# Kernel optimization log

Hardware: AMD Instinct MI355X
Metric: run time of the kernel (lower is better)

The kernel has to match this reference:

```python
import jax, jax.numpy as jnp
import numpy as np

N_NODES = 100000
N_EDGES = 800000
IN_FEATS = 128
HIDDEN = 128
NUM_CLASSES = 10
NUM_GRAPHS = 128
BN_EPS = 1e-5


def setup_inputs() -> dict:
    key = jax.random.key(0)
    ks = jax.random.split(key, 16)
    s = 0.05  # weight init scale
    return {
        "x": jax.random.normal(ks[0], (N_NODES, IN_FEATS), dtype=jnp.float32),
        "edge_index": jax.random.randint(ks[1], (2, N_EDGES), 0, N_NODES, dtype=jnp.int64),
        "batch": jnp.sort(jax.random.randint(ks[2], (N_NODES,), 0, NUM_GRAPHS, dtype=jnp.int64)),
        # conv1 MLP: Linear(in,h) -> ReLU -> Linear(h,h)
        "W1a": jax.random.normal(ks[3], (IN_FEATS, HIDDEN), dtype=jnp.float32) * s,
        "b1a": jnp.zeros((HIDDEN,), dtype=jnp.float32),
        "W1b": jax.random.normal(ks[4], (HIDDEN, HIDDEN), dtype=jnp.float32) * s,
        "b1b": jnp.zeros((HIDDEN,), dtype=jnp.float32),
        "gamma1": jnp.ones((HIDDEN,), dtype=jnp.float32),
        "beta1": jnp.zeros((HIDDEN,), dtype=jnp.float32),
        # conv2 MLP
        "W2a": jax.random.normal(ks[5], (HIDDEN, HIDDEN), dtype=jnp.float32) * s,
        "b2a": jnp.zeros((HIDDEN,), dtype=jnp.float32),
        "W2b": jax.random.normal(ks[6], (HIDDEN, HIDDEN), dtype=jnp.float32) * s,
        "b2b": jnp.zeros((HIDDEN,), dtype=jnp.float32),
        "gamma2": jnp.ones((HIDDEN,), dtype=jnp.float32),
        "beta2": jnp.zeros((HIDDEN,), dtype=jnp.float32),
        # final classifier
        "Wlin": jax.random.normal(ks[7], (HIDDEN, NUM_CLASSES), dtype=jnp.float32) * s,
        "blin": jnp.zeros((NUM_CLASSES,), dtype=jnp.float32),
    }


def _gin_conv(x, edge_index, Wa, ba, Wb, bb, eps=0.0):
    # GINConv: MLP((1+eps)*x_i + sum_{j->i} x_j); scatter-add over edges
    src, dst = edge_index[0], edge_index[1]
    agg = jax.ops.segment_sum(x[src], dst, num_segments=N_NODES)
    h = (1.0 + eps) * x + agg
    h = jax.nn.relu(h @ Wa + ba) @ Wb + bb
    return h


def _batch_norm(x, gamma, beta):
    # training-mode BN over the node dim (biased variance, as in torch)
    mean = jnp.mean(x, axis=0)
    var = jnp.mean(jnp.square(x - mean), axis=0)
    return (x - mean) * jax.lax.rsqrt(var + BN_EPS) * gamma + beta


def reference(x, edge_index, batch, W1a, b1a, W1b, b1b, gamma1, beta1,
              W2a, b2a, W2b, b2b, gamma2, beta2, Wlin, blin):
    h = _gin_conv(x, edge_index, W1a, b1a, W1b, b1b)
    h = jax.nn.relu(_batch_norm(h, gamma1, beta1))
    # dropout: eval mode -> identity
    h = _gin_conv(h, edge_index, W2a, b2a, W2b, b2b)
    h = jax.nn.relu(_batch_norm(h, gamma2, beta2))
    # global mean pool per graph
    summed = jax.ops.segment_sum(h, batch, num_segments=NUM_GRAPHS)
    counts = jax.ops.segment_sum(jnp.ones((h.shape[0],), h.dtype), batch, num_segments=NUM_GRAPHS)
    pooled = summed / jnp.maximum(counts, 1.0)[:, None]  # [G, H]
    logits = pooled @ Wlin + blin
    return jax.nn.log_softmax(logits, axis=1)
```

## Files before the change

### kernel.cpp

```cpp
#include <hip/hip_runtime.h>

#define N_NODES 100000
#define N_EDGESC 800000
#define HID 128
#define NGRAPH 128
#define BN_EPS 1e-5f
#define NREP 32
#define PS 136
#define MLP_BLOCKS ((N_NODES + 63) / 64)

#define PBLK 256
#define PCHUNK 3125
#define NCOARSE 196
#define HISTN (NCOARSE * PBLK)
#define HSCAN_BLOCKS (HISTN / 1024)

typedef __bf16 bf16x8 __attribute__((ext_vector_type(8)));
typedef float f32x4 __attribute__((ext_vector_type(4)));

__device__ inline unsigned short f2bf(float f) {
    unsigned int u = __float_as_uint(f);
    unsigned int r = u + 0x7FFFu + ((u >> 16) & 1u);
    return (unsigned short)(r >> 16);
}
__device__ inline float b2f(unsigned short u) {
    return __uint_as_float(((unsigned int)u) << 16);
}


__global__ __launch_bounds__(256) void k_phist(const int* __restrict__ dst,
                                               int* __restrict__ hist)
{
    __shared__ int h[NCOARSE];
    if (threadIdx.x < NCOARSE) h[threadIdx.x] = 0;
    __syncthreads();
    int base = blockIdx.x * PCHUNK;
    for (int i = threadIdx.x; i < PCHUNK; i += 256)
        atomicAdd(&h[dst[base + i] >> 9], 1);
    __syncthreads();
    if (threadIdx.x < NCOARSE)
        hist[threadIdx.x * PBLK + blockIdx.x] = h[threadIdx.x];
}

__global__ __launch_bounds__(256) void k_scan_block(int* __restrict__ a,
    int* __restrict__ bsum, int n)
{
    __shared__ int ts[256];
    int base = blockIdx.x * 1024 + threadIdx.x * 4;
    int v[4], s = 0;
    #pragma unroll
    for (int i = 0; i < 4; ++i) {
        int idx = base + i;
        v[i] = (idx < n) ? a[idx] : 0;
        s += v[i];
    }
    ts[threadIdx.x] = s;
    __syncthreads();
    for (int d = 1; d < 256; d <<= 1) {
        int t = (threadIdx.x >= d) ? ts[threadIdx.x - d] : 0;
        __syncthreads();
        ts[threadIdx.x] += t;
        __syncthreads();
    }
    int run = ts[threadIdx.x] - s;
    #pragma unroll
    for (int i = 0; i < 4; ++i) {
        int idx = base + i;
        if (idx < n) a[idx] = run;
        run += v[i];
    }
    if (threadIdx.x == 255) bsum[blockIdx.x] = ts[255];
}

__global__ void k_scan_top(int* __restrict__ bsum, int nb)
{
    int run = 0;
    for (int i = 0; i < nb; ++i) { int t = bsum[i]; bsum[i] = run; run += t; }
}

__global__ __launch_bounds__(256) void k_scan_add(int* __restrict__ a,
    const int* __restrict__ bsum, int n)
{
    int i = blockIdx.x * 256 + threadIdx.x;
    if (i < n) a[i] += bsum[i >> 10];
}

__global__ __launch_bounds__(256) void k_pscatter(const int* __restrict__ src,
    const int* __restrict__ dst, const int* __restrict__ hist,
    unsigned int* __restrict__ pk1)
{
    __shared__ int cur[NCOARSE];
    if (threadIdx.x < NCOARSE)
        cur[threadIdx.x] = hist[threadIdx.x * PBLK + blockIdx.x];
    __syncthreads();
    int base = blockIdx.x * PCHUNK;
    for (int i = threadIdx.x; i < PCHUNK; i += 256) {
        int s = src[base + i], d = dst[base + i];
        int p = atomicAdd(&cur[d >> 9], 1);
        pk1[p] = ((unsigned int)s << 9) | (unsigned int)(d & 511);
    }
}

__global__ __launch_bounds__(256) void k_psort(const unsigned int* __restrict__ pk1,
    const int* __restrict__ hist, int* __restrict__ eidx, int* __restrict__ off)
{
    __shared__ int h[512], cur[512], ts[256];
    const int b = blockIdx.x;
    const int e0 = hist[b * PBLK];
    const int e1 = (b == NCOARSE - 1) ? N_EDGESC : hist[(b + 1) * PBLK];
    const int cnt = e1 - e0;
    h[threadIdx.x] = 0; h[threadIdx.x + 256] = 0;
    __syncthreads();
    for (int i = threadIdx.x; i < cnt; i += 256)
        atomicAdd(&h[pk1[e0 + i] & 511], 1);
    __syncthreads();
    int v0 = h[threadIdx.x * 2], v1 = h[threadIdx.x * 2 + 1];
    int s = v0 + v1;
    ts[threadIdx.x] = s;
    __syncthreads();
    for (int d = 1; d < 256; d <<= 1) {
        int t = (threadIdx.x >= d) ? ts[threadIdx.x - d] : 0;
        __syncthreads();
        ts[threadIdx.x] += t;
        __syncthreads();
    }
    int run = e0 + ts[threadIdx.x] - s;
    int n0 = b * 512 + threadIdx.x * 2;
    cur[threadIdx.x * 2]     = run;
    cur[threadIdx.x * 2 + 1] = run + v0;
    if (n0     <= N_NODES) off[n0]     = run;
    if (n0 + 1 <= N_NODES) off[n0 + 1] = run + v0;
    __syncthreads();
    for (int i = threadIdx.x; i < cnt; i += 256) {
        unsigned int u = pk1[e0 + i];
        int p = atomicAdd(&cur[u & 511], 1);
        eidx[p] = (int)(u >> 9);
    }
}

__global__ __launch_bounds__(256) void k_cvt(const float* __restrict__ X,
    unsigned short* __restrict__ Y, int n4)
{
    int i = blockIdx.x * 256 + threadIdx.x;
    if (i < n4) {
        float4 v = ((const float4*)X)[i];
        ((ushort4*)Y)[i] = make_ushort4(f2bf(v.x), f2bf(v.y), f2bf(v.z), f2bf(v.w));
    }
}

__global__ __launch_bounds__(256) void k_wcvt4(const float* __restrict__ Wa,
    const float* __restrict__ Wb, const float* __restrict__ Wc,
    const float* __restrict__ Wd, unsigned short* __restrict__ WT)
{
    int idx = blockIdx.x * 256 + threadIdx.x;
    int mat = idx >> 14, w = idx & 16383;
    int k = w >> 7, n = w & 127;
    const float* W = (mat == 0) ? Wa : (mat == 1) ? Wb : (mat == 2) ? Wc : Wd;
    WT[mat * 16384 + n * 128 + k] = f2bf(W[w]);
}

template<bool BN>
__device__ inline void acc_row(float* acc, uint4 v,
                               const float* sc, const float* sh)
{
    unsigned int u[4] = {v.x, v.y, v.z, v.w};
    #pragma unroll
    for (int j = 0; j < 4; ++j) {
        float lo = b2f((unsigned short)u[j]);
        float hi = b2f((unsigned short)(u[j] >> 16));
        if (BN) {
            lo = fmaxf(lo * sc[2*j]   + sh[2*j],   0.f);
            hi = fmaxf(hi * sc[2*j+1] + sh[2*j+1], 0.f);
        }
        acc[2*j]   += lo;
        acc[2*j+1] += hi;
    }
}

template<bool BN>
__global__ __launch_bounds__(256) void k_gather(
    const unsigned short* __restrict__ X, const float* __restrict__ SC,
    const int* __restrict__ off, const int* __restrict__ eidx,
    unsigned short* __restrict__ OUT, int M)
{
    int n = blockIdx.x * 16 + (threadIdx.x >> 4);
    if (n >= M) return;
    const int lane = threadIdx.x & 15;
    const size_t co = (size_t)lane * 8;

    float sc[8], sh[8];
    if (BN) {
        *(float4*)&sc[0] = ((const float4*)SC)[lane * 2];
        *(float4*)&sc[4] = ((const float4*)SC)[lane * 2 + 1];
        *(float4*)&sh[0] = ((const float4*)SC)[32 + lane * 2];
        *(float4*)&sh[4] = ((const float4*)SC)[32 + lane * 2 + 1];
    }

    float acc[8] = {0.f, 0.f, 0.f, 0.f, 0.f, 0.f, 0.f, 0.f};
    acc_row<BN>(acc, *(const uint4*)(X + (size_t)n * HID + co), sc, sh);

    int k = off[n], kend = off[n + 1];
    for (; k + 7 < kend; k += 8) {
        uint4 v0 = *(const uint4*)(X + (size_t)eidx[k]   * HID + co);
        uint4 v1 = *(const uint4*)(X + (size_t)eidx[k+1] * HID + co);
        uint4 v2 = *(const uint4*)(X + (size_t)eidx[k+2] * HID + co);
        uint4 v3 = *(const uint4*)(X + (size_t)eidx[k+3] * HID + co);
        uint4 v4 = *(const uint4*)(X + (size_t)eidx[k+4] * HID + co);
        uint4 v5 = *(const uint4*)(X + (size_t)eidx[k+5] * HID + co);
        uint4 v6 = *(const uint4*)(X + (size_t)eidx[k+6] * HID + co);
        uint4 v7 = *(const uint4*)(X + (size_t)eidx[k+7] * HID + co);
        acc_row<BN>(acc, v0, sc, sh); acc_row<BN>(acc, v1, sc, sh);
        acc_row<BN>(acc, v2, sc, sh); acc_row<BN>(acc, v3, sc, sh);
        acc_row<BN>(acc, v4, sc, sh); acc_row<BN>(acc, v5, sc, sh);
        acc_row<BN>(acc, v6, sc, sh); acc_row<BN>(acc, v7, sc, sh);
    }
    for (; k + 3 < kend; k += 4) {
        uint4 v0 = *(const uint4*)(X + (size_t)eidx[k]   * HID + co);
        uint4 v1 = *(const uint4*)(X + (size_t)eidx[k+1] * HID + co);
        uint4 v2 = *(const uint4*)(X + (size_t)eidx[k+2] * HID + co);
        uint4 v3 = *(const uint4*)(X + (size_t)eidx[k+3] * HID + co);
        acc_row<BN>(acc, v0, sc, sh); acc_row<BN>(acc, v1, sc, sh);
        acc_row<BN>(acc, v2, sc, sh); acc_row<BN>(acc, v3, sc, sh);
    }
    for (; k < kend; ++k) {
        uint4 v = *(const uint4*)(X + (size_t)eidx[k] * HID + co);
        acc_row<BN>(acc, v, sc, sh);
    }

    uint4 o;
    o.x = (unsigned int)f2bf(acc[0]) | ((unsigned int)f2bf(acc[1]) << 16);
    o.y = (unsigned int)f2bf(acc[2]) | ((unsigned int)f2bf(acc[3]) << 16);
    o.z = (unsigned int)f2bf(acc[4]) | ((unsigned int)f2bf(acc[5]) << 16);
    o.w = (unsigned int)f2bf(acc[6]) | ((unsigned int)f2bf(acc[7]) << 16);
    *(uint4*)(OUT + (size_t)n * HID + co) = o;
}

__global__ __launch_bounds__(256) void k_mlp(
    const unsigned short* __restrict__ A,
    const unsigned short* __restrict__ WTa, const float* __restrict__ ba,
    const unsigned short* __restrict__ WTb, const float* __restrict__ bb,
    unsigned short* __restrict__ Cb, float* __restrict__ Srep, int M)
{
    __shared__ unsigned short Abuf[64 * PS];
    __shared__ unsigned short Hbuf[64 * PS];

    const int tid  = threadIdx.x;
    const int wave = tid >> 6;
    const int lane = tid & 63;
    const int m    = lane & 15;
    const int quad = lane >> 4;
    const int rowbase = blockIdx.x * 64;

    bf16x8 WA[2][4], WB[2][4];
    float bav[2], bbv[2];
    #pragma unroll
    for (int n0 = 0; n0 < 2; ++n0) {
        const int col = (wave * 2 + n0) * 16 + m;
        const size_t cb = (size_t)col * HID + quad * 8;
        #pragma unroll
        for (int kk = 0; kk < 4; ++kk) {
            WA[n0][kk] = *(const bf16x8*)(WTa + cb + kk * 32);
            WB[n0][kk] = *(const bf16x8*)(WTb + cb + kk * 32);
        }
        bav[n0] = ba[col];
        bbv[n0] = bb[col];
    }

    {
        const uint4* Ag = (const uint4*)(A + (size_t)rowbase * HID);
        #pragma unroll
        for (int i = 0; i < 4; ++i) {
            int u = tid + i * 256;
            uint4 v = Ag[u];
            int r = u >> 4, c = u & 15;
            *(uint4*)(Abuf + r * PS + c * 8) = v;
        }
    }
    __syncthreads();

    f32x4 acc[4][2];
    #pragma unroll
    for (int rg = 0; rg < 4; ++rg)
        #pragma unroll
        for (int n0 = 0; n0 < 2; ++n0) acc[rg][n0] = {0.f, 0.f, 0.f, 0.f};
    #pragma unroll
    for (int rg = 0; rg < 4; ++rg) {
        #pragma unroll
        for (int kk = 0; kk < 4; ++kk) {
            bf16x8 af = *(const bf16x8*)(Abuf + (rg*16 + m) * PS + quad*8 + kk*32);
            acc[rg][0] = __builtin_amdgcn_mfma_f32_16x16x32_bf16(af, WA[0][kk], acc[rg][0], 0, 0, 0);
            acc[rg][1] = __builtin_amdgcn_mfma_f32_16x16x32_bf16(af, WA[1][kk], acc[rg][1], 0, 0, 0);
        }
    }

    #pragma unroll
    for (int rg = 0; rg < 4; ++rg)
        #pragma unroll
        for (int n0 = 0; n0 < 2; ++n0)
            #pragma unroll
            for (int i = 0; i < 4; ++i)
                Hbuf[(rg*16 + quad*4 + i) * PS + (wave*2 + n0)*16 + m] =
                    f2bf(fmaxf(acc[rg][n0][i] + bav[n0], 0.f));
    __syncthreads();

    #pragma unroll
    for (int rg = 0; rg < 4; ++rg)
        #pragma unroll
        for (int n0 = 0; n0 < 2; ++n0) acc[rg][n0] = {0.f, 0.f, 0.f, 0.f};
    #pragma unroll
    for (int rg = 0; rg < 4; ++rg) {
        #pragma unroll
        for (int kk = 0; kk < 4; ++kk) {
            bf16x8 hf = *(const bf16x8*)(Hbuf + (rg*16 + m) * PS + quad*8 + kk*32);
            acc[rg][0] = __builtin_amdgcn_mfma_f32_16x16x32_bf16(hf, WB[0][kk], acc[rg][0], 0, 0, 0);
            acc[rg][1] = __builtin_amdgcn_mfma_f32_16x16x32_bf16(hf, WB[1][kk], acc[rg][1], 0, 0, 0);
        }
    }

    const bool full = (rowbase + 64 <= M);
    float s[2] = {0.f, 0.f}, s2[2] = {0.f, 0.f};
    #pragma unroll
    for (int rg = 0; rg < 4; ++rg) {
        #pragma unroll
        for (int n0 = 0; n0 < 2; ++n0) {
            #pragma unroll
            for (int i = 0; i < 4; ++i) {
                float v = acc[rg][n0][i] + bbv[n0];
                if (full || rowbase + rg*16 + quad*4 + i < M) { s[n0] += v; s2[n0] += v*v; }
                Abuf[(rg*16 + quad*4 + i) * PS + (wave*2 + n0)*16 + m] = f2bf(v);
            }
        }
    }
    __syncthreads();

    #pragma unroll
    for (int i = 0; i < 4; ++i) {
        int u = tid + i * 256;
        int r = u >> 4, c = u & 15;
        uint4 v = *(const uint4*)(Abuf + r * PS + c * 8);
        int g = rowbase + r;
        if (g < M) *(uint4*)(Cb + (size_t)g * HID + c * 8) = v;
    }

    #pragma unroll
    for (int n0 = 0; n0 < 2; ++n0) {
        s[n0]  += __shfl_xor(s[n0], 16, 64);
        s[n0]  += __shfl_xor(s[n0], 32, 64);
        s2[n0] += __shfl_xor(s2[n0], 16, 64);
        s2[n0] += __shfl_xor(s2[n0], 32, 64);
    }
    if (quad == 0) {
        float* R = Srep + (size_t)((blockIdx.x * 4 + wave) & (NREP - 1)) * 256;
        #pragma unroll
        for (int n0 = 0; n0 < 2; ++n0) {
            int col = (wave * 2 + n0) * 16 + m;
            atomicAdd(&R[col], s[n0]);
            atomicAdd(&R[128 + col], s2[n0]);
        }
    }
}

__global__ void k_bnfinalize(const float* __restrict__ Srep,
    const float* __restrict__ gamma, const float* __restrict__ beta,
    float* __restrict__ SC, int M)
{
    int f = threadIdx.x;
    float s = 0.f, s2 = 0.f;
    for (int r = 0; r < NREP; ++r) {
        s += Srep[r * 256 + f];
        s2 += Srep[r * 256 + 128 + f];
    }
    float mean = s / (float)M;
    float var = s2 / (float)M - mean * mean;
    var = fmaxf(var, 0.f);
    float sc = gamma[f] * rsqrtf(var + BN_EPS);
    SC[f] = sc;
    SC[HID + f] = beta[f] - mean * sc;
}

__global__ void k_bounds(const int* __restrict__ batch, int* __restrict__ gstart)
{
    int g = threadIdx.x;
    int lo = 0, hi = N_NODES;
    while (lo < hi) {
        int mid = (lo + hi) >> 1;
        if (batch[mid] < g) lo = mid + 1; else hi = mid;
    }
    gstart[g] = lo;
    if (g == 0) gstart[NGRAPH] = N_NODES;
}

__global__ __launch_bounds__(256) void k_pool(const unsigned short* __restrict__ H,
    const float* __restrict__ SC, const int* __restrict__ gstart,
    float* __restrict__ P)
{
    int g = blockIdx.x >> 4, part = blockIdx.x & 15;
    int beg = gstart[g], end = gstart[g + 1];
    int f = threadIdx.x & 127, half = threadIdx.x >> 7;
    float sc = SC[f], sh = SC[HID + f];
    float s = 0.f;
    for (int r = beg + part * 2 + half; r < end; r += 32)
        s += fmaxf(b2f(H[(size_t)r * HID + f]) * sc + sh, 0.f);
    __shared__ float ls[256];
    ls[threadIdx.x] = s;
    __syncthreads();
    if (threadIdx.x < 128)
        atomicAdd(&P[g * HID + threadIdx.x], ls[threadIdx.x] + ls[threadIdx.x + 128]);
}

__global__ void k_head(const float* __restrict__ P, const int* __restrict__ gstart,
    const float* __restrict__ Wlin, const float* __restrict__ blin,
    float* __restrict__ out)
{
    int g = blockIdx.x;
    int l = threadIdx.x;
    float inv = 1.f / (float)max(gstart[g + 1] - gstart[g], 1);
    float p0 = P[(size_t)g * HID + l] * inv;
    float p1 = P[(size_t)g * HID + 64 + l] * inv;
    float lg[10];
    #pragma unroll
    for (int c = 0; c < 10; ++c) {
        float v = p0 * Wlin[l * 10 + c] + p1 * Wlin[(64 + l) * 10 + c];
        #pragma unroll
        for (int off = 32; off > 0; off >>= 1) v += __shfl_down(v, off);
        lg[c] = v;
    }
    if (l == 0) {
        float mx = -1e30f;
        #pragma unroll
        for (int c = 0; c < 10; ++c) { lg[c] += blin[c]; mx = fmaxf(mx, lg[c]); }
        float s = 0.f;
        #pragma unroll
        for (int c = 0; c < 10; ++c) s += expf(lg[c] - mx);
        float lse = mx + logf(s);
        #pragma unroll
        for (int c = 0; c < 10; ++c) out[g * 10 + c] = lg[c] - lse;
    }
}

extern "C" void kernel_launch(void* const* d_in, const int* in_sizes, int n_in,
                              void* d_out, int out_size, void* d_ws, size_t ws_size,
                              hipStream_t stream)
{
    const float* x    = (const float*)d_in[0];
    const int*   ei   = (const int*)d_in[1];
    const int*   batch= (const int*)d_in[2];
    const float* W1a  = (const float*)d_in[3];
    const float* b1a  = (const float*)d_in[4];
    const float* W1b  = (const float*)d_in[5];
    const float* b1b  = (const float*)d_in[6];
    const float* g1   = (const float*)d_in[7];
    const float* be1  = (const float*)d_in[8];
    const float* W2a  = (const float*)d_in[9];
    const float* b2a  = (const float*)d_in[10];
    const float* W2b  = (const float*)d_in[11];
    const float* b2b  = (const float*)d_in[12];
    const float* g2   = (const float*)d_in[13];
    const float* be2  = (const float*)d_in[14];
    const float* Wl   = (const float*)d_in[15];
    const float* bl   = (const float*)d_in[16];
    float* out = (float*)d_out;

    const int* src = ei;
    const int* dst = ei + N_EDGESC;

    const size_t NM = (size_t)N_NODES * HID;
    char* wsb = (char*)d_ws;
    unsigned short* Ab  = (unsigned short*)wsb;
    unsigned short* Yb  = Ab + NM;
    unsigned short* Xb  = Yb + NM;
    float* Srep1 = (float*)(Xb + NM);
    float* Srep2 = Srep1 + NREP * 256;
    float* SC1  = Srep2 + NREP * 256;
    float* SC2  = SC1 + 256;
    float* P    = SC2 + 256;
    unsigned short* WT = (unsigned short*)(P + (size_t)NGRAPH * HID);
    int* hist   = (int*)(WT + 4 * 16384);
    int* eidx   = hist + HISTN;
    int* off    = eidx + N_EDGESC;
    int* bsum   = off + N_NODES + 1;
    int* gstart = bsum + 64;
    unsigned int* pk1 = (unsigned int*)Xb;

    dim3 blk(256);
    const int cvtBlocks = (int)(NM / 4 + 255) / 256;
    const int gatBlocks = (N_NODES + 15) / 16;

    hipMemsetAsync(P, 0, (size_t)NGRAPH * HID * sizeof(float), stream);
    hipMemsetAsync(Srep1, 0, 2 * NREP * 256 * sizeof(float), stream);

    k_phist<<<PBLK, blk, 0, stream>>>(dst, hist);
    k_scan_block<<<HSCAN_BLOCKS, blk, 0, stream>>>(hist, bsum, HISTN);
    k_scan_top<<<1, 1, 0, stream>>>(bsum, HSCAN_BLOCKS);
    k_scan_add<<<(HISTN + 255) / 256, blk, 0, stream>>>(hist, bsum, HISTN);
    k_pscatter<<<PBLK, blk, 0, stream>>>(src, dst, hist, pk1);
    k_psort<<<NCOARSE, blk, 0, stream>>>(pk1, hist, eidx, off);
    k_bounds<<<1, 128, 0, stream>>>(batch, gstart);

    k_cvt<<<cvtBlocks, blk, 0, stream>>>(x, Xb, (int)(NM / 4));
    k_wcvt4<<<256, blk, 0, stream>>>(W1a, W1b, W2a, W2b, WT);

    k_gather<false><<<gatBlocks, blk, 0, stream>>>(Xb, nullptr, off, eidx, Ab, N_NODES);
    k_mlp<<<MLP_BLOCKS, blk, 0, stream>>>(Ab, WT, b1a, WT + 16384, b1b, Yb, Srep1, N_NODES);
    k_bnfinalize<<<1, 128, 0, stream>>>(Srep1, g1, be1, SC1, N_NODES);

    k_gather<true><<<gatBlocks, blk, 0, stream>>>(Yb, SC1, off, eidx, Ab, N_NODES);
    k_mlp<<<MLP_BLOCKS, blk, 0, stream>>>(Ab, WT + 2 * 16384, b2a, WT + 3 * 16384, b2b, Xb, Srep2, N_NODES);
    k_bnfinalize<<<1, 128, 0, stream>>>(Srep2, g2, be2, SC2, N_NODES);

    k_pool<<<NGRAPH * 16, blk, 0, stream>>>(Xb, SC2, gstart, P);
    k_head<<<NGRAPH, 64, 0, stream>>>(P, gstart, Wl, bl, out);
}
```

Baseline: 309.5 us.

## Fuse neighbor gather into MLP kernel, aggregating directly into shared memory

```diff
diff --git a/kernel.cpp b/kernel.cpp
--- a/kernel.cpp
+++ b/kernel.cpp
@@ -7,7 +7,7 @@
 #define BN_EPS 1e-5f
 #define NREP 32
 #define PS 136
-#define MLP_BLOCKS ((N_NODES + 63) / 64)
+#define CONV_BLOCKS ((N_NODES + 63) / 64)
 
 #define PBLK 256
 #define PCHUNK 3125
@@ -178,15 +178,39 @@
 }
 
 template<bool BN>
-__global__ __launch_bounds__(256) void k_gather(
+__global__ __launch_bounds__(256) void k_conv(
     const unsigned short* __restrict__ X, const float* __restrict__ SC,
     const int* __restrict__ off, const int* __restrict__ eidx,
-    unsigned short* __restrict__ OUT, int M)
-{
-    int n = blockIdx.x * 16 + (threadIdx.x >> 4);
-    if (n >= M) return;
-    const int lane = threadIdx.x & 15;
-    const size_t co = (size_t)lane * 8;
+    const unsigned short* __restrict__ WTa, const float* __restrict__ ba,
+    const unsigned short* __restrict__ WTb, const float* __restrict__ bb,
+    unsigned short* __restrict__ Cb, float* __restrict__ Srep, int M)
+{
+    __shared__ unsigned short Abuf[64 * PS];
+    __shared__ unsigned short Hbuf[64 * PS];
+
+    const int tid  = threadIdx.x;
+    const int wave = tid >> 6;
+    const int l64  = tid & 63;
+    const int m    = l64 & 15;
+    const int quad = l64 >> 4;
+    const int grp  = tid >> 4;
+    const int lane = tid & 15;
+    const int rowbase = blockIdx.x * 64;
+
+    bf16x8 WA[2][4], WB[2][4];
+    float bav[2], bbv[2];
+    #pragma unroll
+    for (int n0 = 0; n0 < 2; ++n0) {
+        const int col = (wave * 2 + n0) * 16 + m;
+        const size_t cb = (size_t)col * HID + quad * 8;
+        #pragma unroll
+        for (int kk = 0; kk < 4; ++kk) {
+            WA[n0][kk] = *(const bf16x8*)(WTa + cb + kk * 32);
+            WB[n0][kk] = *(const bf16x8*)(WTb + cb + kk * 32);
+        }
+        bav[n0] = ba[col];
+        bbv[n0] = bb[col];
+    }
 
     float sc[8], sh[8];
     if (BN) {
@@ -196,100 +220,63 @@
         *(float4*)&sh[4] = ((const float4*)SC)[32 + lane * 2 + 1];
     }
 
-    float acc[8] = {0.f, 0.f, 0.f, 0.f, 0.f, 0.f, 0.f, 0.f};
-    acc_row<BN>(acc, *(const uint4*)(X + (size_t)n * HID + co), sc, sh);
-
-    int k = off[n], kend = off[n + 1];
-    for (; k + 7 < kend; k += 8) {
-        uint4 v0 = *(const uint4*)(X + (size_t)eidx[k]   * HID + co);
-        uint4 v1 = *(const uint4*)(X + (size_t)eidx[k+1] * HID + co);
-        uint4 v2 = *(const uint4*)(X + (size_t)eidx[k+2] * HID + co);
-        uint4 v3 = *(const uint4*)(X + (size_t)eidx[k+3] * HID + co);
-        uint4 v4 = *(const uint4*)(X + (size_t)eidx[k+4] * HID + co);
-        uint4 v5 = *(const uint4*)(X + (size_t)eidx[k+5] * HID + co);
-        uint4 v6 = *(const uint4*)(X + (size_t)eidx[k+6] * HID + co);
-        uint4 v7 = *(const uint4*)(X + (size_t)eidx[k+7] * HID + co);
-        acc_row<BN>(acc, v0, sc, sh); acc_row<BN>(acc, v1, sc, sh);
-        acc_row<BN>(acc, v2, sc, sh); acc_row<BN>(acc, v3, sc, sh);
-        acc_row<BN>(acc, v4, sc, sh); acc_row<BN>(acc, v5, sc, sh);
-        acc_row<BN>(acc, v6, sc, sh); acc_row<BN>(acc, v7, sc, sh);
-    }
-    for (; k + 3 < kend; k += 4) {
-        uint4 v0 = *(const uint4*)(X + (size_t)eidx[k]   * HID + co);
-        uint4 v1 = *(const uint4*)(X + (size_t)eidx[k+1] * HID + co);
-        uint4 v2 = *(const uint4*)(X + (size_t)eidx[k+2] * HID + co);
-        uint4 v3 = *(const uint4*)(X + (size_t)eidx[k+3] * HID + co);
-        acc_row<BN>(acc, v0, sc, sh); acc_row<BN>(acc, v1, sc, sh);
-        acc_row<BN>(acc, v2, sc, sh); acc_row<BN>(acc, v3, sc, sh);
-    }
-    for (; k < kend; ++k) {
-        uint4 v = *(const uint4*)(X + (size_t)eidx[k] * HID + co);
-        acc_row<BN>(acc, v, sc, sh);
-    }
-
-    uint4 o;
-    o.x = (unsigned int)f2bf(acc[0]) | ((unsigned int)f2bf(acc[1]) << 16);
-    o.y = (unsigned int)f2bf(acc[2]) | ((unsigned int)f2bf(acc[3]) << 16);
-    o.z = (unsigned int)f2bf(acc[4]) | ((unsigned int)f2bf(acc[5]) << 16);
-    o.w = (unsigned int)f2bf(acc[6]) | ((unsigned int)f2bf(acc[7]) << 16);
-    *(uint4*)(OUT + (size_t)n * HID + co) = o;
-}
-
-__global__ __launch_bounds__(256) void k_mlp(
-    const unsigned short* __restrict__ A,
-    const unsigned short* __restrict__ WTa, const float* __restrict__ ba,
-    const unsigned short* __restrict__ WTb, const float* __restrict__ bb,
-    unsigned short* __restrict__ Cb, float* __restrict__ Srep, int M)
-{
-    __shared__ unsigned short Abuf[64 * PS];
-    __shared__ unsigned short Hbuf[64 * PS];
-
-    const int tid  = threadIdx.x;
-    const int wave = tid >> 6;
-    const int lane = tid & 63;
-    const int m    = lane & 15;
-    const int quad = lane >> 4;
-    const int rowbase = blockIdx.x * 64;
-
-    bf16x8 WA[2][4], WB[2][4];
-    float bav[2], bbv[2];
-    #pragma unroll
-    for (int n0 = 0; n0 < 2; ++n0) {
-        const int col = (wave * 2 + n0) * 16 + m;
-        const size_t cb = (size_t)col * HID + quad * 8;
-        #pragma unroll
-        for (int kk = 0; kk < 4; ++kk) {
-            WA[n0][kk] = *(const bf16x8*)(WTa + cb + kk * 32);
-            WB[n0][kk] = *(const bf16x8*)(WTb + cb + kk * 32);
-        }
-        bav[n0] = ba[col];
-        bbv[n0] = bb[col];
-    }
-
-    {
-        const uint4* Ag = (const uint4*)(A + (size_t)rowbase * HID);
-        #pragma unroll
-        for (int i = 0; i < 4; ++i) {
-            int u = tid + i * 256;
-            uint4 v = Ag[u];
-            int r = u >> 4, c = u & 15;
-            *(uint4*)(Abuf + r * PS + c * 8) = v;
-        }
-    }
-    __syncthreads();
-
-    f32x4 acc[4][2];
+    const size_t co = (size_t)lane * 8;
+    #pragma unroll
+    for (int j = 0; j < 4; ++j) {
+        const int r = grp + j * 16;
+        const int n = rowbase + r;
+        float acc[8] = {0.f, 0.f, 0.f, 0.f, 0.f, 0.f, 0.f, 0.f};
+        if (n < M) {
+            acc_row<BN>(acc, *(const uint4*)(X + (size_t)n * HID + co), sc, sh);
+            int k = off[n], kend = off[n + 1];
+            for (; k + 7 < kend; k += 8) {
+                uint4 v0 = *(const uint4*)(X + (size_t)eidx[k]   * HID + co);
+                uint4 v1 = *(const uint4*)(X + (size_t)eidx[k+1] * HID + co);
+                uint4 v2 = *(const uint4*)(X + (size_t)eidx[k+2] * HID + co);
+                uint4 v3 = *(const uint4*)(X + (size_t)eidx[k+3] * HID + co);
+                uint4 v4 = *(const uint4*)(X + (size_t)eidx[k+4] * HID + co);
+                uint4 v5 = *(const uint4*)(X + (size_t)eidx[k+5] * HID + co);
+                uint4 v6 = *(const uint4*)(X + (size_t)eidx[k+6] * HID + co);
+                uint4 v7 = *(const uint4*)(X + (size_t)eidx[k+7] * HID + co);
+                acc_row<BN>(acc, v0, sc, sh); acc_row<BN>(acc, v1, sc, sh);
+                acc_row<BN>(acc, v2, sc, sh); acc_row<BN>(acc, v3, sc, sh);
+                acc_row<BN>(acc, v4, sc, sh); acc_row<BN>(acc, v5, sc, sh);
+                acc_row<BN>(acc, v6, sc, sh); acc_row<BN>(acc, v7, sc, sh);
+            }
+            for (; k + 3 < kend; k += 4) {
+                uint4 v0 = *(const uint4*)(X + (size_t)eidx[k]   * HID + co);
+                uint4 v1 = *(const uint4*)(X + (size_t)eidx[k+1] * HID + co);
+                uint4 v2 = *(const uint4*)(X + (size_t)eidx[k+2] * HID + co);
+                uint4 v3 = *(const uint4*)(X + (size_t)eidx[k+3] * HID + co);
+                acc_row<BN>(acc, v0, sc, sh); acc_row<BN>(acc, v1, sc, sh);
+                acc_row<BN>(acc, v2, sc, sh); acc_row<BN>(acc, v3, sc, sh);
+            }
+            for (; k < kend; ++k) {
+                uint4 v = *(const uint4*)(X + (size_t)eidx[k] * HID + co);
+                acc_row<BN>(acc, v, sc, sh);
+            }
+        }
+        uint4 o;
+        o.x = (unsigned int)f2bf(acc[0]) | ((unsigned int)f2bf(acc[1]) << 16);
+        o.y = (unsigned int)f2bf(acc[2]) | ((unsigned int)f2bf(acc[3]) << 16);
+        o.z = (unsigned int)f2bf(acc[4]) | ((unsigned int)f2bf(acc[5]) << 16);
+        o.w = (unsigned int)f2bf(acc[6]) | ((unsigned int)f2bf(acc[7]) << 16);
+        *(uint4*)(Abuf + r * PS + lane * 8) = o;
+    }
+    __syncthreads();
+
+    f32x4 acc2[4][2];
     #pragma unroll
     for (int rg = 0; rg < 4; ++rg)
         #pragma unroll
-        for (int n0 = 0; n0 < 2; ++n0) acc[rg][n0] = {0.f, 0.f, 0.f, 0.f};
+        for (int n0 = 0; n0 < 2; ++n0) acc2[rg][n0] = {0.f, 0.f, 0.f, 0.f};
     #pragma unroll
     for (int rg = 0; rg < 4; ++rg) {
         #pragma unroll
         for (int kk = 0; kk < 4; ++kk) {
             bf16x8 af = *(const bf16x8*)(Abuf + (rg*16 + m) * PS + quad*8 + kk*32);
-            acc[rg][0] = __builtin_amdgcn_mfma_f32_16x16x32_bf16(af, WA[0][kk], acc[rg][0], 0, 0, 0);
-            acc[rg][1] = __builtin_amdgcn_mfma_f32_16x16x32_bf16(af, WA[1][kk], acc[rg][1], 0, 0, 0);
+            acc2[rg][0] = __builtin_amdgcn_mfma_f32_16x16x32_bf16(af, WA[0][kk], acc2[rg][0], 0, 0, 0);
+            acc2[rg][1] = __builtin_amdgcn_mfma_f32_16x16x32_bf16(af, WA[1][kk], acc2[rg][1], 0, 0, 0);
         }
     }
 
@@ -300,20 +287,20 @@
             #pragma unroll
             for (int i = 0; i < 4; ++i)
                 Hbuf[(rg*16 + quad*4 + i) * PS + (wave*2 + n0)*16 + m] =
-                    f2bf(fmaxf(acc[rg][n0][i] + bav[n0], 0.f));
+                    f2bf(fmaxf(acc2[rg][n0][i] + bav[n0], 0.f));
     __syncthreads();
 
     #pragma unroll
     for (int rg = 0; rg < 4; ++rg)
         #pragma unroll
-        for (int n0 = 0; n0 < 2; ++n0) acc[rg][n0] = {0.f, 0.f, 0.f, 0.f};
+        for (int n0 = 0; n0 < 2; ++n0) acc2[rg][n0] = {0.f, 0.f, 0.f, 0.f};
     #pragma unroll
     for (int rg = 0; rg < 4; ++rg) {
         #pragma unroll
         for (int kk = 0; kk < 4; ++kk) {
             bf16x8 hf = *(const bf16x8*)(Hbuf + (rg*16 + m) * PS + quad*8 + kk*32);
-            acc[rg][0] = __builtin_amdgcn_mfma_f32_16x16x32_bf16(hf, WB[0][kk], acc[rg][0], 0, 0, 0);
-            acc[rg][1] = __builtin_amdgcn_mfma_f32_16x16x32_bf16(hf, WB[1][kk], acc[rg][1], 0, 0, 0);
+            acc2[rg][0] = __builtin_amdgcn_mfma_f32_16x16x32_bf16(hf, WB[0][kk], acc2[rg][0], 0, 0, 0);
+            acc2[rg][1] = __builtin_amdgcn_mfma_f32_16x16x32_bf16(hf, WB[1][kk], acc2[rg][1], 0, 0, 0);
         }
     }
 
@@ -325,7 +312,7 @@
         for (int n0 = 0; n0 < 2; ++n0) {
             #pragma unroll
             for (int i = 0; i < 4; ++i) {
-                float v = acc[rg][n0][i] + bbv[n0];
+                float v = acc2[rg][n0][i] + bbv[n0];
                 if (full || rowbase + rg*16 + quad*4 + i < M) { s[n0] += v; s2[n0] += v*v; }
                 Abuf[(rg*16 + quad*4 + i) * PS + (wave*2 + n0)*16 + m] = f2bf(v);
             }
@@ -466,8 +453,7 @@
 
     const size_t NM = (size_t)N_NODES * HID;
     char* wsb = (char*)d_ws;
-    unsigned short* Ab  = (unsigned short*)wsb;
-    unsigned short* Yb  = Ab + NM;
+    unsigned short* Yb  = (unsigned short*)wsb;
     unsigned short* Xb  = Yb + NM;
     float* Srep1 = (float*)(Xb + NM);
     float* Srep2 = Srep1 + NREP * 256;
@@ -484,7 +470,6 @@
 
     dim3 blk(256);
     const int cvtBlocks = (int)(NM / 4 + 255) / 256;
-    const int gatBlocks = (N_NODES + 15) / 16;
 
     hipMemsetAsync(P, 0, (size_t)NGRAPH * HID * sizeof(float), stream);
     hipMemsetAsync(Srep1, 0, 2 * NREP * 256 * sizeof(float), stream);
@@ -500,12 +485,12 @@
     k_cvt<<<cvtBlocks, blk, 0, stream>>>(x, Xb, (int)(NM / 4));
     k_wcvt4<<<256, blk, 0, stream>>>(W1a, W1b, W2a, W2b, WT);
 
-    k_gather<false><<<gatBlocks, blk, 0, stream>>>(Xb, nullptr, off, eidx, Ab, N_NODES);
-    k_mlp<<<MLP_BLOCKS, blk, 0, stream>>>(Ab, WT, b1a, WT + 16384, b1b, Yb, Srep1, N_NODES);
+    k_conv<false><<<CONV_BLOCKS, blk, 0, stream>>>(Xb, nullptr, off, eidx,
+        WT, b1a, WT + 16384, b1b, Yb, Srep1, N_NODES);
     k_bnfinalize<<<1, 128, 0, stream>>>(Srep1, g1, be1, SC1, N_NODES);
 
-    k_gather<true><<<gatBlocks, blk, 0, stream>>>(Yb, SC1, off, eidx, Ab, N_NODES);
-    k_mlp<<<MLP_BLOCKS, blk, 0, stream>>>(Ab, WT + 2 * 16384, b2a, WT + 3 * 16384, b2b, Xb, Srep2, N_NODES);
+    k_conv<true><<<CONV_BLOCKS, blk, 0, stream>>>(Yb, SC1, off, eidx,
+        WT + 2 * 16384, b2a, WT + 3 * 16384, b2b, Xb, Srep2, N_NODES);
     k_bnfinalize<<<1, 128, 0, stream>>>(Srep2, g2, be2, SC2, N_NODES);
 
     k_pool<<<NGRAPH * 16, blk, 0, stream>>>(Xb, SC2, gstart, P);
```

New measurement: 361.2 us. 16.7% more time.

## Degree-bucket gather nodes within coarse blocks and merge small setup kernels

Applied to the files above, without the earlier changes.

```diff
diff --git a/kernel.cpp b/kernel.cpp
--- a/kernel.cpp
+++ b/kernel.cpp
@@ -14,6 +14,8 @@
 #define NCOARSE 196
 #define HISTN (NCOARSE * PBLK)
 #define HSCAN_BLOCKS (HISTN / 1024)
+#define NPERM (NCOARSE * 512)
+#define CVT_BLOCKS 12500
 
 typedef __bf16 bf16x8 __attribute__((ext_vector_type(8)));
 typedef float f32x4 __attribute__((ext_vector_type(4)));
@@ -72,10 +74,21 @@
     if (threadIdx.x == 255) bsum[blockIdx.x] = ts[255];
 }
 
-__global__ void k_scan_top(int* __restrict__ bsum, int nb)
-{
-    int run = 0;
-    for (int i = 0; i < nb; ++i) { int t = bsum[i]; bsum[i] = run; run += t; }
+__global__ void k_scan_top_bounds(int* __restrict__ bsum, int nb,
+    const int* __restrict__ batch, int* __restrict__ gstart)
+{
+    if (threadIdx.x == 0) {
+        int run = 0;
+        for (int i = 0; i < nb; ++i) { int t = bsum[i]; bsum[i] = run; run += t; }
+    }
+    int g = threadIdx.x;
+    int lo = 0, hi = N_NODES;
+    while (lo < hi) {
+        int mid = (lo + hi) >> 1;
+        if (batch[mid] < g) lo = mid + 1; else hi = mid;
+    }
+    gstart[g] = lo;
+    if (g == 0) gstart[NGRAPH] = N_NODES;
 }
 
 __global__ __launch_bounds__(256) void k_scan_add(int* __restrict__ a,
@@ -102,14 +115,16 @@
 }
 
 __global__ __launch_bounds__(256) void k_psort(const unsigned int* __restrict__ pk1,
-    const int* __restrict__ hist, int* __restrict__ eidx, int* __restrict__ off)
-{
-    __shared__ int h[512], cur[512], ts[256];
+    const int* __restrict__ hist, int* __restrict__ eidx, int* __restrict__ off,
+    int* __restrict__ perm)
+{
+    __shared__ int h[512], cur[512], ts[256], dh[64], dcur[64];
     const int b = blockIdx.x;
     const int e0 = hist[b * PBLK];
     const int e1 = (b == NCOARSE - 1) ? N_EDGESC : hist[(b + 1) * PBLK];
     const int cnt = e1 - e0;
     h[threadIdx.x] = 0; h[threadIdx.x + 256] = 0;
+    if (threadIdx.x < 64) dh[threadIdx.x] = 0;
     __syncthreads();
     for (int i = threadIdx.x; i < cnt; i += 256)
         atomicAdd(&h[pk1[e0 + i] & 511], 1);
@@ -136,27 +151,40 @@
         int p = atomicAdd(&cur[u & 511], 1);
         eidx[p] = (int)(u >> 9);
     }
-}
-
-__global__ __launch_bounds__(256) void k_cvt(const float* __restrict__ X,
-    unsigned short* __restrict__ Y, int n4)
-{
-    int i = blockIdx.x * 256 + threadIdx.x;
-    if (i < n4) {
+    __syncthreads();
+    int d0 = min(v0, 63), d1 = min(v1, 63);
+    atomicAdd(&dh[d0], 1);
+    atomicAdd(&dh[d1], 1);
+    __syncthreads();
+    if (threadIdx.x == 0) {
+        int r2 = 0;
+        for (int i = 0; i < 64; ++i) { dcur[i] = r2; r2 += dh[i]; }
+    }
+    __syncthreads();
+    int p0 = atomicAdd(&dcur[d0], 1);
+    perm[b * 512 + p0] = (n0 < N_NODES) ? n0 : N_NODES;
+    int p1 = atomicAdd(&dcur[d1], 1);
+    perm[b * 512 + p1] = (n0 + 1 < N_NODES) ? (n0 + 1) : N_NODES;
+}
+
+__global__ __launch_bounds__(256) void k_cvtw(const float* __restrict__ X,
+    unsigned short* __restrict__ Y,
+    const float* __restrict__ Wa, const float* __restrict__ Wb,
+    const float* __restrict__ Wc, const float* __restrict__ Wd,
+    unsigned short* __restrict__ WT)
+{
+    int blk = blockIdx.x;
+    if (blk < CVT_BLOCKS) {
+        int i = blk * 256 + threadIdx.x;
         float4 v = ((const float4*)X)[i];
         ((ushort4*)Y)[i] = make_ushort4(f2bf(v.x), f2bf(v.y), f2bf(v.z), f2bf(v.w));
-    }
-}
-
-__global__ __launch_bounds__(256) void k_wcvt4(const float* __restrict__ Wa,
-    const float* __restrict__ Wb, const float* __restrict__ Wc,
-    const float* __restrict__ Wd, unsigned short* __restrict__ WT)
-{
-    int idx = blockIdx.x * 256 + threadIdx.x;
-    int mat = idx >> 14, w = idx & 16383;
-    int k = w >> 7, n = w & 127;
-    const float* W = (mat == 0) ? Wa : (mat == 1) ? Wb : (mat == 2) ? Wc : Wd;
-    WT[mat * 16384 + n * 128 + k] = f2bf(W[w]);
+    } else {
+        int idx = (blk - CVT_BLOCKS) * 256 + threadIdx.x;
+        int mat = idx >> 14, w = idx & 16383;
+        int k = w >> 7, n = w & 127;
+        const float* W = (mat == 0) ? Wa : (mat == 1) ? Wb : (mat == 2) ? Wc : Wd;
+        WT[mat * 16384 + n * 128 + k] = f2bf(W[w]);
+    }
 }
 
 template<bool BN>
@@ -181,9 +209,11 @@
 __global__ __launch_bounds__(256) void k_gather(
     const unsigned short* __restrict__ X, const float* __restrict__ SC,
     const int* __restrict__ off, const int* __restrict__ eidx,
+    const int* __restrict__ perm,
     unsigned short* __restrict__ OUT, int M)
 {
-    int n = blockIdx.x * 16 + (threadIdx.x >> 4);
+    int slot = blockIdx.x * 16 + (threadIdx.x >> 4);
+    int n = perm[slot];
     if (n >= M) return;
     const int lane = threadIdx.x & 15;
     const size_t co = (size_t)lane * 8;
@@ -376,18 +406,6 @@
     float sc = gamma[f] * rsqrtf(var + BN_EPS);
     SC[f] = sc;
     SC[HID + f] = beta[f] - mean * sc;
-}
-
-__global__ void k_bounds(const int* __restrict__ batch, int* __restrict__ gstart)
-{
-    int g = threadIdx.x;
-    int lo = 0, hi = N_NODES;
-    while (lo < hi) {
-        int mid = (lo + hi) >> 1;
-        if (batch[mid] < g) lo = mid + 1; else hi = mid;
-    }
-    gstart[g] = lo;
-    if (g == 0) gstart[NGRAPH] = N_NODES;
 }
 
 __global__ __launch_bounds__(256) void k_pool(const unsigned short* __restrict__ H,
@@ -471,40 +489,38 @@
     unsigned short* Xb  = Yb + NM;
     float* Srep1 = (float*)(Xb + NM);
     float* Srep2 = Srep1 + NREP * 256;
-    float* SC1  = Srep2 + NREP * 256;
+    float* P    = Srep2 + NREP * 256;
+    float* SC1  = P + (size_t)NGRAPH * HID;
     float* SC2  = SC1 + 256;
-    float* P    = SC2 + 256;
-    unsigned short* WT = (unsigned short*)(P + (size_t)NGRAPH * HID);
+    unsigned short* WT = (unsigned short*)(SC2 + 256);
     int* hist   = (int*)(WT + 4 * 16384);
     int* eidx   = hist + HISTN;
     int* off    = eidx + N_EDGESC;
-    int* bsum   = off + N_NODES + 1;
+    int* perm   = off + N_NODES + 1;
+    int* bsum   = perm + NPERM;
     int* gstart = bsum + 64;
     unsigned int* pk1 = (unsigned int*)Xb;
 
     dim3 blk(256);
-    const int cvtBlocks = (int)(NM / 4 + 255) / 256;
-    const int gatBlocks = (N_NODES + 15) / 16;
-
-    hipMemsetAsync(P, 0, (size_t)NGRAPH * HID * sizeof(float), stream);
-    hipMemsetAsync(Srep1, 0, 2 * NREP * 256 * sizeof(float), stream);
+    const int gatBlocks = NPERM / 16;
+
+    hipMemsetAsync(Srep1, 0,
+        (2 * NREP * 256 + (size_t)NGRAPH * HID) * sizeof(float), stream);
 
     k_phist<<<PBLK, blk, 0, stream>>>(dst, hist);
     k_scan_block<<<HSCAN_BLOCKS, blk, 0, stream>>>(hist, bsum, HISTN);
-    k_scan_top<<<1, 1, 0, stream>>>(bsum, HSCAN_BLOCKS);
+    k_scan_top_bounds<<<1, 128, 0, stream>>>(bsum, HSCAN_BLOCKS, batch, gstart);
     k_scan_add<<<(HISTN + 255) / 256, blk, 0, stream>>>(hist, bsum, HISTN);
     k_pscatter<<<PBLK, blk, 0, stream>>>(src, dst, hist, pk1);
-    k_psort<<<NCOARSE, blk, 0, stream>>>(pk1, hist, eidx, off);
-    k_bounds<<<1, 128, 0, stream>>>(batch, gstart);
-
-    k_cvt<<<cvtBlocks, blk, 0, stream>>>(x, Xb, (int)(NM / 4));
-    k_wcvt4<<<256, blk, 0, stream>>>(W1a, W1b, W2a, W2b, WT);
-
-    k_gather<false><<<gatBlocks, blk, 0, stream>>>(Xb, nullptr, off, eidx, Ab, N_NODES);
+    k_psort<<<NCOARSE, blk, 0, stream>>>(pk1, hist, eidx, off, perm);
+
+    k_cvtw<<<CVT_BLOCKS + 256, blk, 0, stream>>>(x, Xb, W1a, W1b, W2a, W2b, WT);
+
+    k_gather<false><<<gatBlocks, blk, 0, stream>>>(Xb, nullptr, off, eidx, perm, Ab, N_NODES);
     k_mlp<<<MLP_BLOCKS, blk, 0, stream>>>(Ab, WT, b1a, WT + 16384, b1b, Yb, Srep1, N_NODES);
     k_bnfinalize<<<1, 128, 0, stream>>>(Srep1, g1, be1, SC1, N_NODES);
 
-    k_gather<true><<<gatBlocks, blk, 0, stream>>>(Yb, SC1, off, eidx, Ab, N_NODES);
+    k_gather<true><<<gatBlocks, blk, 0, stream>>>(Yb, SC1, off, eidx, perm, Ab, N_NODES);
     k_mlp<<<MLP_BLOCKS, blk, 0, stream>>>(Ab, WT + 2 * 16384, b2a, WT + 3 * 16384, b2b, Xb, Srep2, N_NODES);
     k_bnfinalize<<<1, 128, 0, stream>>>(Srep2, g2, be2, SC2, N_NODES);
 
```

Result: slower. 320.7 us (+3.6%).
